# Kernel optimization log

Measured on AMD Instinct MI355X. Metric: run time of the kernel, lower is better.

Reference implementation:

```python
import jax, jax.numpy as jnp
import numpy as np

SIGMA = 25.0
B = 4096            # number of graphs
N = 1048576         # total nodes across batch
FEAT = 44           # node feature dim
TED = 84            # t_embed_dim = 128 - 44


def setup_inputs() -> dict:
    key = jax.random.key(0)
    ks = jax.random.split(key, 12)
    # ragged graph sizes via sorted random cut points -> ptr of length B+1
    cuts = jnp.sort(jax.random.randint(ks[0], (B - 1,), 0, N))
    ptr = jnp.concatenate([jnp.zeros((1,), jnp.int32), cuts.astype(jnp.int32), jnp.full((1,), N, jnp.int32)])
    node_attr = jax.random.normal(ks[1], (N, FEAT), dtype=jnp.float32)
    t = jax.random.uniform(ks[2], (B,), dtype=jnp.float32, minval=1e-3, maxval=1.0)
    # GaussianFourierProjection buffer (requires_grad=False in torch)
    W_f = jax.random.normal(ks[3], (TED // 2,), dtype=jnp.float32) * 30.0
    # embed Linear 84->84
    embed_w = jax.random.normal(ks[4], (TED, TED), dtype=jnp.float32) / np.sqrt(TED)
    embed_b = jax.random.normal(ks[5], (TED,), dtype=jnp.float32) * 0.01
    # Linear chain 128->64->32->4 (torch convention: W [out, in])
    w0 = jax.random.normal(ks[6], (64, 128), dtype=jnp.float32) / np.sqrt(128)
    b0 = jax.random.normal(ks[7], (64,), dtype=jnp.float32) * 0.01
    w1 = jax.random.normal(ks[8], (32, 64), dtype=jnp.float32) / np.sqrt(64)
    b1 = jax.random.normal(ks[9], (32,), dtype=jnp.float32) * 0.01
    w2 = jax.random.normal(ks[10], (4, 32), dtype=jnp.float32) / np.sqrt(32)
    b2 = jax.random.normal(ks[11], (4,), dtype=jnp.float32) * 0.01
    return {"node_attr": node_attr, "t": t, "ptr": ptr, "W_f": W_f,
            "embed_w": embed_w, "embed_b": embed_b,
            "w0": w0, "b0": b0, "w1": w1, "b1": b1, "w2": w2, "b2": b2}


def reference(node_attr, t, ptr, W_f, embed_w, embed_b, w0, b0, w1, b1, w2, b2):
    swish = lambda x: x * jax.nn.sigmoid(x)
    # GaussianFourierProjection: [B, TED]
    x_proj = t[:, None] * W_f[None, :] * (2.0 * np.pi)
    t_emb = jnp.concatenate([jnp.sin(x_proj), jnp.cos(x_proj)], axis=-1)
    embed = swish(t_emb @ embed_w.T + embed_b)                      # [B, TED]
    # ragged broadcast: graph id per node (replaces the torch per-graph tile loop)
    seg = jnp.searchsorted(ptr, jnp.arange(node_attr.shape[0], dtype=ptr.dtype), side='right') - 1
    h = jnp.concatenate([node_attr, embed[seg]], axis=-1)           # [N, 128]
    h = swish(h @ w0.T + b0)                                        # [N, 64]
    h = swish(h @ w1.T + b1)                                        # [N, 32]
    h = swish(h @ w2.T + b2)                                        # [N, 4]
    std = jnp.sqrt((SIGMA ** (2.0 * t) - 1.0) / (2.0 * np.log(SIGMA)))  # [B]
    return h / std[seg][:, None]
```

## Files before the change

kernel.cpp:

```cpp
#include <hip/hip_runtime.h>
#include <hip/hip_fp16.h>

typedef _Float16 f16x8 __attribute__((ext_vector_type(8)));
typedef __fp16   fp16x2 __attribute__((ext_vector_type(2)));
typedef float f32x4 __attribute__((ext_vector_type(4)));

#define FEAT 44
#define TED  84
#define MT   128
#define WN   32
#define NBLK 768
#define BUFB 6144

__global__ void prep_all(const float* __restrict__ t_arr, const float* __restrict__ W_f,
                         const float* __restrict__ embed_w, const float* __restrict__ embed_b,
                         const float* __restrict__ w0, const float* __restrict__ b0,
                         const float* __restrict__ w1, const float* __restrict__ w2,
                         const int* __restrict__ gptr, int* __restrict__ seg, int do_seg,
                         float* __restrict__ emb0, float* __restrict__ inv_std,
                         _Float16* __restrict__ w0h, _Float16* __restrict__ w1h,
                         _Float16* __restrict__ w2h, int B) {
    int g   = blockIdx.x;
    int tid = threadIdx.x;
    if (g == B) {
        for (int i = tid; i < 64 * 64; i += 128) {
            int o = i >> 6, k = i & 63;
            w0h[i] = (k < FEAT) ? (_Float16)w0[o * 128 + k] : (_Float16)0.f;
        }
        for (int i = tid; i < 32 * 64; i += 128) w1h[i] = (_Float16)w1[i];
        for (int i = tid; i < 16 * 32; i += 128) w2h[i] = (i < 4 * 32) ? (_Float16)w2[i] : (_Float16)0.f;
        return;
    }
    if (do_seg) {
        int a = gptr[g], b = gptr[g + 1];
        for (int i = a + tid; i < b; i += 128) seg[i] = g;
    }
    __shared__ float temb[TED];
    __shared__ float ses[TED];
    float tv = t_arr[g];
    if (tid < TED) {
        int j   = (tid < TED / 2) ? tid : tid - TED / 2;
        float x = tv * W_f[j] * 6.283185307179586f;
        temb[tid] = (tid < TED / 2) ? sinf(x) : cosf(x);
    }
    __syncthreads();
    if (tid < TED) {
        const float* wr = embed_w + tid * TED;
        float s = embed_b[tid];
        #pragma unroll 4
        for (int j = 0; j < TED; ++j) s = fmaf(temb[j], wr[j], s);
        ses[tid] = s / (1.0f + __expf(-s));
    }
    if (tid == TED) {
        const float c = 6.437751649736401f;
        inv_std[g] = rsqrtf(expm1f(c * tv) / c);
    }
    __syncthreads();
    if (tid < 64) {
        const float* wr = w0 + tid * 128 + FEAT;
        float s = b0[tid];
        #pragma unroll 4
        for (int j = 0; j < TED; ++j) s = fmaf(ses[j], wr[j], s);
        emb0[g * 64 + tid] = s;
    }
}

__device__ __forceinline__ float swishf(float x) {
    float e = __builtin_amdgcn_exp2f(x * -1.4426950408889634f);
    return x * __builtin_amdgcn_rcpf(1.0f + e);
}

__device__ __forceinline__ int ubound(const int* __restrict__ p, int n, int v) {
    int lo = 0, hi = n;
    while (lo < hi) { int m = (lo + hi) >> 1; if (p[m] <= v) lo = m + 1; else hi = m; }
    return lo - 1;
}

__device__ __forceinline__ void stage_attr(const float* __restrict__ node_attr, int row0,
                                           const char* lim, char* dst, int lane) {
    const char* g = (const char*)node_attr + (size_t)row0 * (FEAT * 4);
    #pragma unroll
    for (int k = 0; k < 6; ++k) {
        const char* s = g + k * 1024 + lane * 16;
        if (k == 5 && s > lim) s = lim;
        __builtin_amdgcn_global_load_lds(
            (const __attribute__((address_space(1))) unsigned int*)s,
            (__attribute__((address_space(3))) unsigned int*)(dst + k * 1024),
            16, 0, 0);
    }
}

template<bool USE_SEG>
__global__ __launch_bounds__(256)
void scorenet_main(const float* __restrict__ node_attr,
                   const int* __restrict__ gptr, int B,
                   const int* __restrict__ seg_arr,
                   const float* __restrict__ emb0,
                   const float* __restrict__ inv_std_g,
                   const _Float16* __restrict__ w0h,
                   const _Float16* __restrict__ w1h,
                   const _Float16* __restrict__ w2h,
                   const float* __restrict__ b1,
                   const float* __restrict__ b2,
                   float* __restrict__ out, int ntiles, int nbytes_attr) {
    __shared__ __align__(16) char lds[2 * BUFB * 4];

    const int t    = threadIdx.x;
    const int lane = t & 63;
    const int wid  = t >> 6;
    const int lr   = lane & 15;
    const int lk   = lane >> 4;
    const char* lim = (const char*)node_attr + nbytes_attr - 16;

    if (blockIdx.x >= ntiles) return;
    const int stride = gridDim.x;

    f16x8 aw0[2][4];
    #pragma unroll
    for (int kt = 0; kt < 2; ++kt)
        #pragma unroll
        for (int mt = 0; mt < 4; ++mt)
            aw0[kt][mt] = *(const f16x8*)(w0h + (mt * 16 + lr) * 64 + kt * 32 + lk * 8);
    f16x8 aw1[2][2];
    #pragma unroll
    for (int kt = 0; kt < 2; ++kt)
        #pragma unroll
        for (int mt = 0; mt < 2; ++mt)
            aw1[kt][mt] = *(const f16x8*)(w1h + (mt * 16 + lr) * 64 + kt * 32 + lk * 8);
    f16x8 aw2 = *(const f16x8*)(w2h + lr * 32 + lk * 8);
    f32x4 bias1f[2];
    #pragma unroll
    for (int mt = 0; mt < 2; ++mt) {
        float4 bv = *(const float4*)(b1 + mt * 16 + lk * 4);
        bias1f[mt] = f32x4{bv.x, bv.y, bv.z, bv.w};
    }
    float4 b2vv = *(const float4*)b2;
    const f32x4 c2init = (lk == 0) ? f32x4{b2vv.x, b2vv.y, b2vv.z, b2vv.w} : f32x4{0.f, 0.f, 0.f, 0.f};

    char* buf_cur = lds + wid * (2 * BUFB);
    char* buf_nxt = buf_cur + BUFB;

    int tile = blockIdx.x;

    stage_attr(node_attr, tile * MT + wid * WN, lim, buf_cur, lane);
    int s0, s1, n0, n1;
    {
        int wb = tile * MT + wid * WN;
        if (USE_SEG) { s0 = seg_arr[wb + lr]; s1 = seg_arr[wb + 16 + lr]; }
        else { s0 = ubound(gptr, B + 1, wb + lr); s1 = ubound(gptr, B + 1, wb + 16 + lr); }
        int t1 = tile + stride; if (t1 >= ntiles) t1 = tile;
        int wb1 = t1 * MT + wid * WN;
        if (USE_SEG) { n0 = seg_arr[wb1 + lr]; n1 = seg_arr[wb1 + 16 + lr]; }
        else { n0 = ubound(gptr, B + 1, wb1 + lr); n1 = ubound(gptr, B + 1, wb1 + 16 + lr); }
    }

    while (tile < ntiles) {
        const int wb = tile * MT + wid * WN;
        int tp1 = tile + stride;     if (tp1 >= ntiles) tp1 = tile;
        int tp2 = tile + 2 * stride; if (tp2 >= ntiles) tp2 = tile;

        float is0 = inv_std_g[s0];
        float is1 = inv_std_g[s1];
        f32x4 acc0[4][2];
        #pragma unroll
        for (int mt = 0; mt < 4; ++mt) {
            acc0[mt][0] = *(const f32x4*)(emb0 + s0 * 64 + mt * 16 + lk * 4);
            acc0[mt][1] = *(const f32x4*)(emb0 + s1 * 64 + mt * 16 + lk * 4);
        }

        stage_attr(node_attr, tp1 * MT + wid * WN, lim, buf_nxt, lane);

        int m0, m1;
        {
            int wb2 = tp2 * MT + wid * WN;
            if (USE_SEG) { m0 = seg_arr[wb2 + lr]; m1 = seg_arr[wb2 + 16 + lr]; }
            else { m0 = ubound(gptr, B + 1, wb2 + lr); m1 = ubound(gptr, B + 1, wb2 + 16 + lr); }
        }

        asm volatile("s_waitcnt vmcnt(18)" ::: "memory");
        __builtin_amdgcn_sched_barrier(0);

        union u8 { fp16x2 h2[4]; f16x8 v; };
        f16x8 bf[2][2];
        #pragma unroll
        for (int nt = 0; nt < 2; ++nt) {
            const float4* rowp = (const float4*)(buf_cur + (nt * 16 + lr) * (FEAT * 4));
            float4 a = rowp[lk * 2];
            float4 b = rowp[lk * 2 + 1];
            float4 c = make_float4(0.f, 0.f, 0.f, 0.f);
            float4 d = make_float4(0.f, 0.f, 0.f, 0.f);
            if (lk == 0) { c = rowp[8]; d = rowp[9]; }
            else if (lk == 1) { c = rowp[10]; }
            u8 f0, f1;
            f0.h2[0] = __builtin_amdgcn_cvt_pkrtz(a.x, a.y);
            f0.h2[1] = __builtin_amdgcn_cvt_pkrtz(a.z, a.w);
            f0.h2[2] = __builtin_amdgcn_cvt_pkrtz(b.x, b.y);
            f0.h2[3] = __builtin_amdgcn_cvt_pkrtz(b.z, b.w);
            f1.h2[0] = __builtin_amdgcn_cvt_pkrtz(c.x, c.y);
            f1.h2[1] = __builtin_amdgcn_cvt_pkrtz(c.z, c.w);
            f1.h2[2] = __builtin_amdgcn_cvt_pkrtz(d.x, d.y);
            f1.h2[3] = __builtin_amdgcn_cvt_pkrtz(d.z, d.w);
            bf[nt][0] = f0.v;
            bf[nt][1] = f1.v;
        }

        #pragma unroll
        for (int kt = 0; kt < 2; ++kt)
            #pragma unroll
            for (int mt = 0; mt < 4; ++mt)
                #pragma unroll
                for (int nt = 0; nt < 2; ++nt)
                    acc0[mt][nt] = __builtin_amdgcn_mfma_f32_16x16x32_f16(aw0[kt][mt], bf[nt][kt], acc0[mt][nt], 0, 0, 0);

        #pragma unroll
        for (int mt = 0; mt < 4; ++mt)
            #pragma unroll
            for (int nt = 0; nt < 2; ++nt) {
                int j = nt * 16 + lr;
                union { fp16x2 h2[2]; uint2 u; } p;
                p.h2[0] = __builtin_amdgcn_cvt_pkrtz(swishf(acc0[mt][nt][0]), swishf(acc0[mt][nt][1]));
                p.h2[1] = __builtin_amdgcn_cvt_pkrtz(swishf(acc0[mt][nt][2]), swishf(acc0[mt][nt][3]));
                int addr = j * 128 + (mt * 16 + lk * 4) * 2;
                *(uint2*)(buf_cur + (addr ^ ((j & 7) << 4))) = p.u;
            }

        f32x4 acc1[2][2];
        #pragma unroll
        for (int mt = 0; mt < 2; ++mt) { acc1[mt][0] = bias1f[mt]; acc1[mt][1] = bias1f[mt]; }
        #pragma unroll
        for (int kt = 0; kt < 2; ++kt) {
            f16x8 bx[2];
            #pragma unroll
            for (int nt = 0; nt < 2; ++nt) {
                int j    = nt * 16 + lr;
                int addr = j * 128 + kt * 64 + lk * 16;
                bx[nt] = *(const f16x8*)(buf_cur + (addr ^ ((j & 7) << 4)));
            }
            #pragma unroll
            for (int mt = 0; mt < 2; ++mt)
                #pragma unroll
                for (int nt = 0; nt < 2; ++nt)
                    acc1[mt][nt] = __builtin_amdgcn_mfma_f32_16x16x32_f16(aw1[kt][mt], bx[nt], acc1[mt][nt], 0, 0, 0);
        }

        #pragma unroll
        for (int mt = 0; mt < 2; ++mt)
            #pragma unroll
            for (int nt = 0; nt < 2; ++nt) {
                int j = nt * 16 + lr;
                union { fp16x2 h2[2]; uint2 u; } p;
                p.h2[0] = __builtin_amdgcn_cvt_pkrtz(swishf(acc1[mt][nt][0]), swishf(acc1[mt][nt][1]));
                p.h2[1] = __builtin_amdgcn_cvt_pkrtz(swishf(acc1[mt][nt][2]), swishf(acc1[mt][nt][3]));
                int addr = 4096 + j * 64 + (mt * 16 + lk * 4) * 2;
                *(uint2*)(buf_cur + (addr ^ ((j & 3) << 4))) = p.u;
            }

        f32x4 acc2[2] = {c2init, c2init};
        #pragma unroll
        for (int nt = 0; nt < 2; ++nt) {
            int j    = nt * 16 + lr;
            int addr = 4096 + j * 64 + lk * 16;
            f16x8 bx = *(const f16x8*)(buf_cur + (addr ^ ((j & 3) << 4)));
            acc2[nt] = __builtin_amdgcn_mfma_f32_16x16x32_f16(aw2, bx, acc2[nt], 0, 0, 0);
        }
        if (lk == 0) {
            #pragma unroll
            for (int nt = 0; nt < 2; ++nt) {
                int j = nt * 16 + lr;
                float is = nt ? is1 : is0;
                float4 o;
                o.x = swishf(acc2[nt][0]) * is;
                o.y = swishf(acc2[nt][1]) * is;
                o.z = swishf(acc2[nt][2]) * is;
                o.w = swishf(acc2[nt][3]) * is;
                *(float4*)(out + (size_t)(wb + j) * 4) = o;
            }
        }

        { char* tmp = buf_cur; buf_cur = buf_nxt; buf_nxt = tmp; }
        s0 = n0; s1 = n1; n0 = m0; n1 = m1;
        tile += stride;
    }
}

extern "C" void kernel_launch(void* const* d_in, const int* in_sizes, int n_in,
                              void* d_out, int out_size, void* d_ws, size_t ws_size,
                              hipStream_t stream) {
    const float* node_attr = (const float*)d_in[0];
    const float* t_arr     = (const float*)d_in[1];
    const int*   gptr      = (const int*)d_in[2];
    const float* W_f       = (const float*)d_in[3];
    const float* embed_w   = (const float*)d_in[4];
    const float* embed_b   = (const float*)d_in[5];
    const float* w0        = (const float*)d_in[6];
    const float* b0        = (const float*)d_in[7];
    const float* w1        = (const float*)d_in[8];
    const float* b1        = (const float*)d_in[9];
    const float* w2        = (const float*)d_in[10];
    const float* b2        = (const float*)d_in[11];
    float* out = (float*)d_out;

    const int N = in_sizes[0] / FEAT;
    const int B = in_sizes[2] - 1;
    const int ntiles = N / MT;
    const int nbytes_attr = in_sizes[0] * 4;

    char* ws = (char*)d_ws;
    size_t off = 0;
    float*    emb0    = (float*)(ws + off); off += (size_t)B * 64 * sizeof(float);
    off = (off + 1023) & ~(size_t)1023;
    float*    inv_std = (float*)(ws + off); off += (size_t)B * sizeof(float);
    off = (off + 1023) & ~(size_t)1023;
    _Float16* w0h = (_Float16*)(ws + off);  off += 64 * 64 * sizeof(_Float16);
    _Float16* w1h = (_Float16*)(ws + off);  off += 32 * 64 * sizeof(_Float16);
    _Float16* w2h = (_Float16*)(ws + off);  off += 16 * 32 * sizeof(_Float16);
    off = (off + 1023) & ~(size_t)1023;
    int* seg = (int*)(ws + off);
    size_t need_with_seg = off + (size_t)N * sizeof(int);
    bool use_seg = (ws_size >= need_with_seg);

    const int grid = (ntiles < NBLK) ? ntiles : NBLK;

    prep_all<<<B + 1, 128, 0, stream>>>(t_arr, W_f, embed_w, embed_b, w0, b0, w1, w2,
                                        gptr, seg, use_seg ? 1 : 0,
                                        emb0, inv_std, w0h, w1h, w2h, B);
    if (use_seg) {
        scorenet_main<true><<<grid, 256, 0, stream>>>(node_attr, gptr, B, seg, emb0, inv_std,
                                                      w0h, w1h, w2h, b1, b2, out, ntiles, nbytes_attr);
    } else {
        scorenet_main<false><<<grid, 256, 0, stream>>>(node_attr, gptr, B, seg, emb0, inv_std,
                                                       w0h, w1h, w2h, b1, b2, out, ntiles, nbytes_attr);
    }
}
```

Before: 84.76 us.

## Replace static grid-stride tiling with atomic dynamic chunk scheduling

Blocks now grab chunks of four consecutive tiles from a global atomic counter, which prep_all resets, instead of walking a fixed grid stride. Each chunk restarts the double-buffered prefetch pipeline, and the pipeline no longer prefetches across chunk boundaries. The goal is to balance load across blocks and improve locality of consecutive tiles. In exchange it adds an atomic plus two block barriers per chunk and a full vmcnt drain at every chunk start, which exposes load latency.

```diff
diff --git a/kernel.cpp b/kernel.cpp
--- a/kernel.cpp
+++ b/kernel.cpp
@@ -10,6 +10,7 @@
 #define MT   128
 #define WN   32
 #define NBLK 768
+#define CH   4
 #define BUFB 6144
 
 __global__ void prep_all(const float* __restrict__ t_arr, const float* __restrict__ W_f,
@@ -19,10 +20,11 @@
                          const int* __restrict__ gptr, int* __restrict__ seg, int do_seg,
                          float* __restrict__ emb0, float* __restrict__ inv_std,
                          _Float16* __restrict__ w0h, _Float16* __restrict__ w1h,
-                         _Float16* __restrict__ w2h, int B) {
+                         _Float16* __restrict__ w2h, int* __restrict__ tile_ctr, int B) {
     int g   = blockIdx.x;
     int tid = threadIdx.x;
     if (g == B) {
+        if (tid == 0) tile_ctr[0] = 0;
         for (int i = tid; i < 64 * 64; i += 128) {
             int o = i >> 6, k = i & 63;
             w0h[i] = (k < FEAT) ? (_Float16)w0[o * 128 + k] : (_Float16)0.f;
@@ -102,8 +104,10 @@
                    const _Float16* __restrict__ w2h,
                    const float* __restrict__ b1,
                    const float* __restrict__ b2,
+                   int* __restrict__ tile_ctr,
                    float* __restrict__ out, int ntiles, int nbytes_attr) {
     __shared__ __align__(16) char lds[2 * BUFB * 4];
+    __shared__ int chunk_s;
 
     const int t    = threadIdx.x;
     const int lane = t & 63;
@@ -111,9 +115,7 @@
     const int lr   = lane & 15;
     const int lk   = lane >> 4;
     const char* lim = (const char*)node_attr + nbytes_attr - 16;
-
-    if (blockIdx.x >= ntiles) return;
-    const int stride = gridDim.x;
+    const int nchunks = (ntiles + CH - 1) / CH;
 
     f16x8 aw0[2][4];
     #pragma unroll
@@ -140,146 +142,158 @@
     char* buf_cur = lds + wid * (2 * BUFB);
     char* buf_nxt = buf_cur + BUFB;
 
-    int tile = blockIdx.x;
-
-    stage_attr(node_attr, tile * MT + wid * WN, lim, buf_cur, lane);
-    int s0, s1, n0, n1;
-    {
-        int wb = tile * MT + wid * WN;
-        if (USE_SEG) { s0 = seg_arr[wb + lr]; s1 = seg_arr[wb + 16 + lr]; }
-        else { s0 = ubound(gptr, B + 1, wb + lr); s1 = ubound(gptr, B + 1, wb + 16 + lr); }
-        int t1 = tile + stride; if (t1 >= ntiles) t1 = tile;
-        int wb1 = t1 * MT + wid * WN;
-        if (USE_SEG) { n0 = seg_arr[wb1 + lr]; n1 = seg_arr[wb1 + 16 + lr]; }
-        else { n0 = ubound(gptr, B + 1, wb1 + lr); n1 = ubound(gptr, B + 1, wb1 + 16 + lr); }
-    }
-
-    while (tile < ntiles) {
-        const int wb = tile * MT + wid * WN;
-        int tp1 = tile + stride;     if (tp1 >= ntiles) tp1 = tile;
-        int tp2 = tile + 2 * stride; if (tp2 >= ntiles) tp2 = tile;
-
-        float is0 = inv_std_g[s0];
-        float is1 = inv_std_g[s1];
-        f32x4 acc0[4][2];
-        #pragma unroll
-        for (int mt = 0; mt < 4; ++mt) {
-            acc0[mt][0] = *(const f32x4*)(emb0 + s0 * 64 + mt * 16 + lk * 4);
-            acc0[mt][1] = *(const f32x4*)(emb0 + s1 * 64 + mt * 16 + lk * 4);
+    while (true) {
+        if (t == 0) chunk_s = atomicAdd(tile_ctr, 1);
+        __syncthreads();
+        const int c = chunk_s;
+        __syncthreads();
+        if (c >= nchunks) break;
+        const int t0   = c * CH;
+        const int cend = (t0 + CH < ntiles) ? t0 + CH : ntiles;
+
+        asm volatile("s_waitcnt vmcnt(0)" ::: "memory");
+        __builtin_amdgcn_sched_barrier(0);
+
+        int s0, s1, n0, n1;
+        {
+            int wb = t0 * MT + wid * WN;
+            if (USE_SEG) { s0 = seg_arr[wb + lr]; s1 = seg_arr[wb + 16 + lr]; }
+            else { s0 = ubound(gptr, B + 1, wb + lr); s1 = ubound(gptr, B + 1, wb + 16 + lr); }
         }
-
-        stage_attr(node_attr, tp1 * MT + wid * WN, lim, buf_nxt, lane);
-
-        int m0, m1;
+        stage_attr(node_attr, t0 * MT + wid * WN, lim, buf_cur, lane);
         {
-            int wb2 = tp2 * MT + wid * WN;
-            if (USE_SEG) { m0 = seg_arr[wb2 + lr]; m1 = seg_arr[wb2 + 16 + lr]; }
-            else { m0 = ubound(gptr, B + 1, wb2 + lr); m1 = ubound(gptr, B + 1, wb2 + 16 + lr); }
+            int t1 = (t0 + 1 < cend) ? t0 + 1 : cend - 1;
+            int wb1 = t1 * MT + wid * WN;
+            if (USE_SEG) { n0 = seg_arr[wb1 + lr]; n1 = seg_arr[wb1 + 16 + lr]; }
+            else { n0 = ubound(gptr, B + 1, wb1 + lr); n1 = ubound(gptr, B + 1, wb1 + 16 + lr); }
         }
 
-        asm volatile("s_waitcnt vmcnt(18)" ::: "memory");
-        __builtin_amdgcn_sched_barrier(0);
-
-        union u8 { fp16x2 h2[4]; f16x8 v; };
-        f16x8 bf[2][2];
-        #pragma unroll
-        for (int nt = 0; nt < 2; ++nt) {
-            const float4* rowp = (const float4*)(buf_cur + (nt * 16 + lr) * (FEAT * 4));
-            float4 a = rowp[lk * 2];
-            float4 b = rowp[lk * 2 + 1];
-            float4 c = make_float4(0.f, 0.f, 0.f, 0.f);
-            float4 d = make_float4(0.f, 0.f, 0.f, 0.f);
-            if (lk == 0) { c = rowp[8]; d = rowp[9]; }
-            else if (lk == 1) { c = rowp[10]; }
-            u8 f0, f1;
-            f0.h2[0] = __builtin_amdgcn_cvt_pkrtz(a.x, a.y);
-            f0.h2[1] = __builtin_amdgcn_cvt_pkrtz(a.z, a.w);
-            f0.h2[2] = __builtin_amdgcn_cvt_pkrtz(b.x, b.y);
-            f0.h2[3] = __builtin_amdgcn_cvt_pkrtz(b.z, b.w);
-            f1.h2[0] = __builtin_amdgcn_cvt_pkrtz(c.x, c.y);
-            f1.h2[1] = __builtin_amdgcn_cvt_pkrtz(c.z, c.w);
-            f1.h2[2] = __builtin_amdgcn_cvt_pkrtz(d.x, d.y);
-            f1.h2[3] = __builtin_amdgcn_cvt_pkrtz(d.z, d.w);
-            bf[nt][0] = f0.v;
-            bf[nt][1] = f1.v;
-        }
-
-        #pragma unroll
-        for (int kt = 0; kt < 2; ++kt)
+        for (int tile = t0; tile < cend; ++tile) {
+            const int wb = tile * MT + wid * WN;
+            int tp1 = tile + 1; if (tp1 >= cend) tp1 = cend - 1;
+            int tp2 = tile + 2; if (tp2 >= cend) tp2 = cend - 1;
+
+            float is0 = inv_std_g[s0];
+            float is1 = inv_std_g[s1];
+            f32x4 acc0[4][2];
+            #pragma unroll
+            for (int mt = 0; mt < 4; ++mt) {
+                acc0[mt][0] = *(const f32x4*)(emb0 + s0 * 64 + mt * 16 + lk * 4);
+                acc0[mt][1] = *(const f32x4*)(emb0 + s1 * 64 + mt * 16 + lk * 4);
+            }
+
+            stage_attr(node_attr, tp1 * MT + wid * WN, lim, buf_nxt, lane);
+
+            int m0, m1;
+            {
+                int wb2 = tp2 * MT + wid * WN;
+                if (USE_SEG) { m0 = seg_arr[wb2 + lr]; m1 = seg_arr[wb2 + 16 + lr]; }
+                else { m0 = ubound(gptr, B + 1, wb2 + lr); m1 = ubound(gptr, B + 1, wb2 + 16 + lr); }
+            }
+
+            asm volatile("s_waitcnt vmcnt(20)" ::: "memory");
+            __builtin_amdgcn_sched_barrier(0);
+
+            union u8 { fp16x2 h2[4]; f16x8 v; };
+            f16x8 bf[2][2];
+            #pragma unroll
+            for (int nt = 0; nt < 2; ++nt) {
+                const float4* rowp = (const float4*)(buf_cur + (nt * 16 + lr) * (FEAT * 4));
+                float4 a = rowp[lk * 2];
+                float4 b = rowp[lk * 2 + 1];
+                float4 c4 = make_float4(0.f, 0.f, 0.f, 0.f);
+                float4 d = make_float4(0.f, 0.f, 0.f, 0.f);
+                if (lk == 0) { c4 = rowp[8]; d = rowp[9]; }
+                else if (lk == 1) { c4 = rowp[10]; }
+                u8 f0, f1;
+                f0.h2[0] = __builtin_amdgcn_cvt_pkrtz(a.x, a.y);
+                f0.h2[1] = __builtin_amdgcn_cvt_pkrtz(a.z, a.w);
+                f0.h2[2] = __builtin_amdgcn_cvt_pkrtz(b.x, b.y);
+                f0.h2[3] = __builtin_amdgcn_cvt_pkrtz(b.z, b.w);
+                f1.h2[0] = __builtin_amdgcn_cvt_pkrtz(c4.x, c4.y);
+                f1.h2[1] = __builtin_amdgcn_cvt_pkrtz(c4.z, c4.w);
+                f1.h2[2] = __builtin_amdgcn_cvt_pkrtz(d.x, d.y);
+                f1.h2[3] = __builtin_amdgcn_cvt_pkrtz(d.z, d.w);
+                bf[nt][0] = f0.v;
+                bf[nt][1] = f1.v;
+            }
+
+            #pragma unroll
+            for (int kt = 0; kt < 2; ++kt)
+                #pragma unroll
+                for (int mt = 0; mt < 4; ++mt)
+                    #pragma unroll
+                    for (int nt = 0; nt < 2; ++nt)
+                        acc0[mt][nt] = __builtin_amdgcn_mfma_f32_16x16x32_f16(aw0[kt][mt], bf[nt][kt], acc0[mt][nt], 0, 0, 0);
+
             #pragma unroll
             for (int mt = 0; mt < 4; ++mt)
                 #pragma unroll
-                for (int nt = 0; nt < 2; ++nt)
-                    acc0[mt][nt] = __builtin_amdgcn_mfma_f32_16x16x32_f16(aw0[kt][mt], bf[nt][kt], acc0[mt][nt], 0, 0, 0);
-
-        #pragma unroll
-        for (int mt = 0; mt < 4; ++mt)
-            #pragma unroll
-            for (int nt = 0; nt < 2; ++nt) {
-                int j = nt * 16 + lr;
-                union { fp16x2 h2[2]; uint2 u; } p;
-                p.h2[0] = __builtin_amdgcn_cvt_pkrtz(swishf(acc0[mt][nt][0]), swishf(acc0[mt][nt][1]));
-                p.h2[1] = __builtin_amdgcn_cvt_pkrtz(swishf(acc0[mt][nt][2]), swishf(acc0[mt][nt][3]));
-                int addr = j * 128 + (mt * 16 + lk * 4) * 2;
-                *(uint2*)(buf_cur + (addr ^ ((j & 7) << 4))) = p.u;
-            }
-
-        f32x4 acc1[2][2];
-        #pragma unroll
-        for (int mt = 0; mt < 2; ++mt) { acc1[mt][0] = bias1f[mt]; acc1[mt][1] = bias1f[mt]; }
-        #pragma unroll
-        for (int kt = 0; kt < 2; ++kt) {
-            f16x8 bx[2];
+                for (int nt = 0; nt < 2; ++nt) {
+                    int j = nt * 16 + lr;
+                    union { fp16x2 h2[2]; uint2 u; } p;
+                    p.h2[0] = __builtin_amdgcn_cvt_pkrtz(swishf(acc0[mt][nt][0]), swishf(acc0[mt][nt][1]));
+                    p.h2[1] = __builtin_amdgcn_cvt_pkrtz(swishf(acc0[mt][nt][2]), swishf(acc0[mt][nt][3]));
+                    int addr = j * 128 + (mt * 16 + lk * 4) * 2;
+                    *(uint2*)(buf_cur + (addr ^ ((j & 7) << 4))) = p.u;
+                }
+
+            f32x4 acc1[2][2];
+            #pragma unroll
+            for (int mt = 0; mt < 2; ++mt) { acc1[mt][0] = bias1f[mt]; acc1[mt][1] = bias1f[mt]; }
+            #pragma unroll
+            for (int kt = 0; kt < 2; ++kt) {
+                f16x8 bx[2];
+                #pragma unroll
+                for (int nt = 0; nt < 2; ++nt) {
+                    int j    = nt * 16 + lr;
+                    int addr = j * 128 + kt * 64 + lk * 16;
+                    bx[nt] = *(const f16x8*)(buf_cur + (addr ^ ((j & 7) << 4)));
+                }
+                #pragma unroll
+                for (int mt = 0; mt < 2; ++mt)
+                    #pragma unroll
+                    for (int nt = 0; nt < 2; ++nt)
+                        acc1[mt][nt] = __builtin_amdgcn_mfma_f32_16x16x32_f16(aw1[kt][mt], bx[nt], acc1[mt][nt], 0, 0, 0);
+            }
+
+            #pragma unroll
+            for (int mt = 0; mt < 2; ++mt)
+                #pragma unroll
+                for (int nt = 0; nt < 2; ++nt) {
+                    int j = nt * 16 + lr;
+                    union { fp16x2 h2[2]; uint2 u; } p;
+                    p.h2[0] = __builtin_amdgcn_cvt_pkrtz(swishf(acc1[mt][nt][0]), swishf(acc1[mt][nt][1]));
+                    p.h2[1] = __builtin_amdgcn_cvt_pkrtz(swishf(acc1[mt][nt][2]), swishf(acc1[mt][nt][3]));
+                    int addr = 4096 + j * 64 + (mt * 16 + lk * 4) * 2;
+                    *(uint2*)(buf_cur + (addr ^ ((j & 3) << 4))) = p.u;
+                }
+
+            f32x4 acc2[2] = {c2init, c2init};
             #pragma unroll
             for (int nt = 0; nt < 2; ++nt) {
                 int j    = nt * 16 + lr;
-                int addr = j * 128 + kt * 64 + lk * 16;
-                bx[nt] = *(const f16x8*)(buf_cur + (addr ^ ((j & 7) << 4)));
-            }
-            #pragma unroll
-            for (int mt = 0; mt < 2; ++mt)
-                #pragma unroll
-                for (int nt = 0; nt < 2; ++nt)
-                    acc1[mt][nt] = __builtin_amdgcn_mfma_f32_16x16x32_f16(aw1[kt][mt], bx[nt], acc1[mt][nt], 0, 0, 0);
+                int addr = 4096 + j * 64 + lk * 16;
+                f16x8 bx = *(const f16x8*)(buf_cur + (addr ^ ((j & 3) << 4)));
+                acc2[nt] = __builtin_amdgcn_mfma_f32_16x16x32_f16(aw2, bx, acc2[nt], 0, 0, 0);
+            }
+            if (lk == 0) {
+                #pragma unroll
+                for (int nt = 0; nt < 2; ++nt) {
+                    int j = nt * 16 + lr;
+                    float is = nt ? is1 : is0;
+                    float4 o;
+                    o.x = swishf(acc2[nt][0]) * is;
+                    o.y = swishf(acc2[nt][1]) * is;
+                    o.z = swishf(acc2[nt][2]) * is;
+                    o.w = swishf(acc2[nt][3]) * is;
+                    *(float4*)(out + (size_t)(wb + j) * 4) = o;
+                }
+            }
+
+            { char* tmp = buf_cur; buf_cur = buf_nxt; buf_nxt = tmp; }
+            s0 = n0; s1 = n1; n0 = m0; n1 = m1;
         }
-
-        #pragma unroll
-        for (int mt = 0; mt < 2; ++mt)
-            #pragma unroll
-            for (int nt = 0; nt < 2; ++nt) {
-                int j = nt * 16 + lr;
-                union { fp16x2 h2[2]; uint2 u; } p;
-                p.h2[0] = __builtin_amdgcn_cvt_pkrtz(swishf(acc1[mt][nt][0]), swishf(acc1[mt][nt][1]));
-                p.h2[1] = __builtin_amdgcn_cvt_pkrtz(swishf(acc1[mt][nt][2]), swishf(acc1[mt][nt][3]));
-                int addr = 4096 + j * 64 + (mt * 16 + lk * 4) * 2;
-                *(uint2*)(buf_cur + (addr ^ ((j & 3) << 4))) = p.u;
-            }
-
-        f32x4 acc2[2] = {c2init, c2init};
-        #pragma unroll
-        for (int nt = 0; nt < 2; ++nt) {
-            int j    = nt * 16 + lr;
-            int addr = 4096 + j * 64 + lk * 16;
-            f16x8 bx = *(const f16x8*)(buf_cur + (addr ^ ((j & 3) << 4)));
-            acc2[nt] = __builtin_amdgcn_mfma_f32_16x16x32_f16(aw2, bx, acc2[nt], 0, 0, 0);
-        }
-        if (lk == 0) {
-            #pragma unroll
-            for (int nt = 0; nt < 2; ++nt) {
-                int j = nt * 16 + lr;
-                float is = nt ? is1 : is0;
-                float4 o;
-                o.x = swishf(acc2[nt][0]) * is;
-                o.y = swishf(acc2[nt][1]) * is;
-                o.z = swishf(acc2[nt][2]) * is;
-                o.w = swishf(acc2[nt][3]) * is;
-                *(float4*)(out + (size_t)(wb + j) * 4) = o;
-            }
-        }
-
-        { char* tmp = buf_cur; buf_cur = buf_nxt; buf_nxt = tmp; }
-        s0 = n0; s1 = n1; n0 = m0; n1 = m1;
-        tile += stride;
     }
 }
 
@@ -315,20 +329,22 @@
     _Float16* w1h = (_Float16*)(ws + off);  off += 32 * 64 * sizeof(_Float16);
     _Float16* w2h = (_Float16*)(ws + off);  off += 16 * 32 * sizeof(_Float16);
     off = (off + 1023) & ~(size_t)1023;
+    int* tile_ctr = (int*)(ws + off);       off += 1024;
     int* seg = (int*)(ws + off);
     size_t need_with_seg = off + (size_t)N * sizeof(int);
     bool use_seg = (ws_size >= need_with_seg);
 
-    const int grid = (ntiles < NBLK) ? ntiles : NBLK;
+    const int nchunks = (ntiles + CH - 1) / CH;
+    const int grid = (nchunks < NBLK) ? nchunks : NBLK;
 
     prep_all<<<B + 1, 128, 0, stream>>>(t_arr, W_f, embed_w, embed_b, w0, b0, w1, w2,
                                         gptr, seg, use_seg ? 1 : 0,
-                                        emb0, inv_std, w0h, w1h, w2h, B);
+                                        emb0, inv_std, w0h, w1h, w2h, tile_ctr, B);
     if (use_seg) {
         scorenet_main<true><<<grid, 256, 0, stream>>>(node_attr, gptr, B, seg, emb0, inv_std,
-                                                      w0h, w1h, w2h, b1, b2, out, ntiles, nbytes_attr);
+                                                      w0h, w1h, w2h, b1, b2, tile_ctr, out, ntiles, nbytes_attr);
     } else {
         scorenet_main<false><<<grid, 256, 0, stream>>>(node_attr, gptr, B, seg, emb0, inv_std,
-                                                       w0h, w1h, w2h, b1, b2, out, ntiles, nbytes_attr);
-    }
-}
+                                                       w0h, w1h, w2h, b1, b2, tile_ctr, out, ntiles, nbytes_attr);
+    }
+}
```

New measurement: 89.32 us. 1.05x slower.
